# Kernel tuning notes

Measured on AMD Instinct MI355X. Metric: run time of the kernel, lower is better.

## Reference

```python
import jax, jax.numpy as jnp
import numpy as np

B, C, H, W = 8, 256, 64, 64
CI = 128  # inter_channels
EPS = 1e-5

def conv1x1(x, w, b):
    # x:[B,C,H,W], w:[O,C], b:[O] -> [B,O,H,W]
    return jnp.einsum('bchw,oc->bohw', x, w) + b[None, :, None, None]

def maxpool2(t):
    b, c, h, w = t.shape
    return t.reshape(b, c, h // 2, 2, w // 2, 2).max(axis=(3, 5))

def setup_inputs() -> dict:
    key = jax.random.key(0)
    ks = jax.random.split(key, 11)
    s_in = 1.0 / np.sqrt(C)
    s_ci = 1.0 / np.sqrt(CI)
    return {
        'x':        jax.random.normal(ks[0], (B, C, H, W), jnp.float32),
        'g_w':      jax.random.normal(ks[1], (CI, C), jnp.float32) * s_in,
        'g_b':      jax.random.normal(ks[2], (CI,), jnp.float32) * s_in,
        'theta_w':  jax.random.normal(ks[3], (CI, C), jnp.float32) * s_in,
        'theta_b':  jax.random.normal(ks[4], (CI,), jnp.float32) * s_in,
        'phi_w':    jax.random.normal(ks[5], (CI, C), jnp.float32) * s_in,
        'phi_b':    jax.random.normal(ks[6], (CI,), jnp.float32) * s_in,
        'w_w':      jax.random.normal(ks[7], (C, CI), jnp.float32) * s_ci,
        'w_b':      jax.random.normal(ks[8], (C,), jnp.float32) * s_ci,
        'bn_gamma': jax.random.normal(ks[9], (C,), jnp.float32) * 0.1 + 1.0,
        'bn_beta':  jax.random.normal(ks[10], (C,), jnp.float32) * 0.1,
    }

def reference(x, g_w, g_b, theta_w, theta_b, phi_w, phi_b, w_w, w_b, bn_gamma, bn_beta):
    b, c, h, w = x.shape
    n = h * w
    # g and phi are sub-sampled with 2x2 max pool -> Ns = n // 4
    g_x = maxpool2(conv1x1(x, g_w, g_b)).reshape(b, CI, -1)      # [B,CI,Ns]
    g_x = g_x.transpose(0, 2, 1)                                  # [B,Ns,CI]
    theta_x = conv1x1(x, theta_w, theta_b).reshape(b, CI, n)
    theta_x = theta_x.transpose(0, 2, 1)                          # [B,N,CI]
    phi_x = maxpool2(conv1x1(x, phi_w, phi_b)).reshape(b, CI, -1)  # [B,CI,Ns]
    f = jnp.einsum('bnc,bcm->bnm', theta_x, phi_x)                # [B,N,Ns] (no 1/sqrt(d) scale, faithful)
    f_div_c = jax.nn.softmax(f, axis=-1)
    y = jnp.einsum('bnm,bmc->bnc', f_div_c, g_x)                  # [B,N,CI]
    y = y.transpose(0, 2, 1).reshape(b, CI, h, w)
    wy = conv1x1(y, w_w, w_b)                                     # [B,C,H,W]
    # BatchNorm2d in training mode: batch stats over (B,H,W)
    mean = wy.mean(axis=(0, 2, 3), keepdims=True)
    var = wy.var(axis=(0, 2, 3), keepdims=True)
    wy_bn = (wy - mean) * jax.lax.rsqrt(var + EPS)
    wy_bn = wy_bn * bn_gamma[None, :, None, None] + bn_beta[None, :, None, None]
    return wy_bn + x
```

## Files before the change

### kernel.cpp

```cpp
#include <hip/hip_runtime.h>
#include <hip/hip_bf16.h>
#include <hip/hip_fp16.h>
#include <math.h>

#define B 8
#define C 256
#define HH 64
#define WW 64
#define NN 4096
#define CI 128
#define NS 1024
#define EPS 1e-5f

typedef __attribute__((ext_vector_type(8))) _Float16 f16x8;
typedef __attribute__((ext_vector_type(4))) float f32x4;

static __device__ __forceinline__ unsigned short f2h_bits(float f) {
    return __half_as_ushort(__float2half(f));
}
static __device__ __forceinline__ float h2f(unsigned short u) {
    return __half2float(__ushort_as_half(u));
}

__global__ __launch_bounds__(256) void k_xt(const float* __restrict__ x,
        unsigned short* __restrict__ xh,
        const float* __restrict__ tw, const float* __restrict__ pw,
        const float* __restrict__ gw, const float* __restrict__ ww,
        unsigned short* __restrict__ wh) {
    int tid = threadIdx.x;
    if (blockIdx.x == 64) {
        int inst = blockIdx.y * B + blockIdx.z;
        int base = inst * 4096;
        #pragma unroll
        for (int k = 0; k < 16; ++k) {
            int idx = base + tid + k * 256;
            int sel = idx >> 15, off = idx & 32767;
            const float* src = (sel == 0) ? tw : (sel == 1) ? pw : (sel == 2) ? gw : ww;
            wh[idx] = f2h_bits(src[off]);
        }
        return;
    }
    __shared__ float s_t[64 * 65];
    int n0 = blockIdx.x * 64;
    int c0 = blockIdx.y * 64;
    int b  = blockIdx.z;
    #pragma unroll
    for (int k = 0; k < 16; ++k) {
        int idx = tid + k * 256;
        int cl = idx >> 6, nl = idx & 63;
        s_t[cl * 65 + nl] = x[((size_t)b * C + c0 + cl) * NN + n0 + nl];
    }
    __syncthreads();
    #pragma unroll
    for (int k = 0; k < 8; ++k) {
        int idx = tid + k * 256;
        int nl = idx >> 5, cp = (idx & 31) * 2;
        ushort2 o;
        o.x = f2h_bits(s_t[cp * 65 + nl]);
        o.y = f2h_bits(s_t[(cp + 1) * 65 + nl]);
        *(ushort2*)&xh[((size_t)b * NN + n0 + nl) * C + c0 + cp] = o;
    }
}

__global__ __launch_bounds__(512) void k_convs(const unsigned short* __restrict__ xh,
        const unsigned short* __restrict__ twh, const unsigned short* __restrict__ pwh,
        const unsigned short* __restrict__ gwh,
        const float* __restrict__ tb, const float* __restrict__ pb, const float* __restrict__ gb_,
        unsigned short* __restrict__ theta, unsigned short* __restrict__ phi,
        unsigned short* __restrict__ gout) {
    int blk = blockIdx.x;
    int b   = blk >> 5;
    int mh  = blk & 31;
    int tid = threadIdx.x;
    int lane = tid & 63, wv = tid >> 6;
    int lr = lane & 15, lh = lane >> 4;
    int wn = wv & 3, wc = wv >> 2;
    size_t row0 = (size_t)blk * 128;

    f32x4 accT[8];
    f32x4 aP0[4], aP1[4], aG0[4], aG1[4];
    #pragma unroll
    for (int i = 0; i < 8; ++i) accT[i] = (f32x4){0,0,0,0};
    #pragma unroll
    for (int i = 0; i < 4; ++i) {
        aP0[i] = (f32x4){0,0,0,0}; aP1[i] = (f32x4){0,0,0,0};
        aG0[i] = (f32x4){0,0,0,0}; aG1[i] = (f32x4){0,0,0,0};
    }

    const unsigned short* ap0 = xh + (row0 + wn * 16 + lr) * C + lh * 8;
    const unsigned short* ap1 = ap0 + (size_t)64 * C;
    #pragma unroll
    for (int kc = 0; kc < 8; ++kc) {
        f16x8 a0 = *(const f16x8*)(ap0 + kc * 32);
        f16x8 a1 = *(const f16x8*)(ap1 + kc * 32);
        f16x8 aT = (wv < 4) ? a0 : a1;
        #pragma unroll
        for (int ct = 0; ct < 8; ++ct) {
            f16x8 bt_ = *(const f16x8*)&twh[(ct * 16 + lr) * C + kc * 32 + lh * 8];
            accT[ct] = __builtin_amdgcn_mfma_f32_16x16x32_f16(aT, bt_, accT[ct], 0, 0, 0);
        }
        #pragma unroll
        for (int ct = 0; ct < 4; ++ct) {
            int wrow = (wc * 64 + ct * 16 + lr) * C + kc * 32 + lh * 8;
            f16x8 bp = *(const f16x8*)&pwh[wrow];
            f16x8 bg = *(const f16x8*)&gwh[wrow];
            aP0[ct] = __builtin_amdgcn_mfma_f32_16x16x32_f16(a0, bp, aP0[ct], 0, 0, 0);
            aP1[ct] = __builtin_amdgcn_mfma_f32_16x16x32_f16(a1, bp, aP1[ct], 0, 0, 0);
            aG0[ct] = __builtin_amdgcn_mfma_f32_16x16x32_f16(a0, bg, aG0[ct], 0, 0, 0);
            aG1[ct] = __builtin_amdgcn_mfma_f32_16x16x32_f16(a1, bg, aG1[ct], 0, 0, 0);
        }
    }
    #pragma unroll
    for (int ct = 0; ct < 8; ++ct) {
        int ci = ct * 16 + lr;
        float bias = tb[ci];
        #pragma unroll
        for (int r = 0; r < 4; ++r)
            theta[(row0 + wv * 16 + lh * 4 + r) * CI + ci] = f2h_bits(accT[ct][r] + bias);
    }
    #pragma unroll
    for (int ct = 0; ct < 4; ++ct) {
        int ci = wc * 64 + ct * 16 + lr;
        float biasP = pb[ci], biasG = gb_[ci];
        #pragma unroll
        for (int j = 0; j < 2; ++j) {
            int m = mh * 32 + wn * 8 + lh * 2 + j;
            float vP = fmaxf(fmaxf(aP0[ct][2*j], aP0[ct][2*j+1]),
                             fmaxf(aP1[ct][2*j], aP1[ct][2*j+1])) + biasP;
            float vG = fmaxf(fmaxf(aG0[ct][2*j], aG0[ct][2*j+1]),
                             fmaxf(aG1[ct][2*j], aG1[ct][2*j+1])) + biasG;
            phi[((size_t)b * NS + m) * CI + ci]  = f2h_bits(vP);
            gout[((size_t)b * CI + ci) * NS + m] = f2h_bits(vG);
        }
    }
}

#define SPH 136
#define SG  72
#define SP  68
__global__ __launch_bounds__(256) void k_attn_mfma(const unsigned short* __restrict__ theta,
        const unsigned short* __restrict__ phi, const unsigned short* __restrict__ g,
        unsigned short* __restrict__ y) {
    __shared__ unsigned short s_ph[2][64 * SPH];
    __shared__ unsigned short s_g[2][128 * SG];
    __shared__ unsigned short s_p[64 * SP];
    int rb = blockIdx.x;
    int b  = blockIdx.y;
    int tid = threadIdx.x;
    int lane = tid & 63, wv = tid >> 6;
    int lr = lane & 15, lh = lane >> 4;
    int row0 = rb * 64;
    int wrow = wv * 16;

    f16x8 a_th[4];
    {
        const unsigned short* tp = theta + ((size_t)b * NN + row0 + wrow + lr) * CI + lh * 8;
        #pragma unroll
        for (int kc = 0; kc < 4; ++kc) a_th[kc] = *(const f16x8*)(tp + kc * 32);
    }

    const ushort4* phsrc = (const ushort4*)(phi + (size_t)b * NS * CI);
    const ushort4* gsrc  = (const ushort4*)(g + (size_t)b * CI * NS);

    f32x4 yacc[8];
    #pragma unroll
    for (int i = 0; i < 8; ++i) yacc[i] = (f32x4){0.f, 0.f, 0.f, 0.f};
    float mrun[4] = {-1e30f, -1e30f, -1e30f, -1e30f};
    float lrun[4] = {0.f, 0.f, 0.f, 0.f};

    ushort4 rph[8], rg[8];
    #pragma unroll
    for (int k = 0; k < 8; ++k) {
        int t = tid + k * 256;
        rph[k] = phsrc[(t >> 5) * 32 + (t & 31)];
        rg[k]  = gsrc[(t >> 4) * 256 + (t & 15)];
    }
    #pragma unroll
    for (int k = 0; k < 8; ++k) {
        int t = tid + k * 256;
        *(ushort4*)&s_ph[0][(t >> 5) * SPH + (t & 31) * 4] = rph[k];
        *(ushort4*)&s_g[0][(t >> 4) * SG + (t & 15) * 4]   = rg[k];
    }
    __syncthreads();
    int cur = 0;

    for (int mt = 0; mt < 16; ++mt) {
        if (mt < 15) {
            #pragma unroll
            for (int k = 0; k < 8; ++k) {
                int t = tid + k * 256;
                rph[k] = phsrc[((mt + 1) * 64 + (t >> 5)) * 32 + (t & 31)];
                rg[k]  = gsrc[(t >> 4) * 256 + (mt + 1) * 16 + (t & 15)];
            }
        }
        const unsigned short* ph = s_ph[cur];
        const unsigned short* sg_ = s_g[cur];

        f32x4 S[4];
        #pragma unroll
        for (int nt = 0; nt < 4; ++nt) S[nt] = (f32x4){0.f, 0.f, 0.f, 0.f};
        __builtin_amdgcn_s_setprio(1);
        #pragma unroll
        for (int nt = 0; nt < 4; ++nt) {
            #pragma unroll
            for (int kc = 0; kc < 4; ++kc) {
                f16x8 bf = *(const f16x8*)&ph[(nt * 16 + lr) * SPH + kc * 32 + lh * 8];
                S[nt] = __builtin_amdgcn_mfma_f32_16x16x32_f16(a_th[kc], bf, S[nt], 0, 0, 0);
            }
        }
        __builtin_amdgcn_s_setprio(0);

        float rmax[4], rs[4], scale[4];
        #pragma unroll
        for (int r = 0; r < 4; ++r)
            rmax[r] = fmaxf(fmaxf(S[0][r], S[1][r]), fmaxf(S[2][r], S[3][r]));
        #pragma unroll
        for (int s = 1; s < 16; s <<= 1) {
            #pragma unroll
            for (int r = 0; r < 4; ++r) rmax[r] = fmaxf(rmax[r], __shfl_xor(rmax[r], s));
        }
        #pragma unroll
        for (int r = 0; r < 4; ++r) {
            float mnew = fmaxf(mrun[r], rmax[r]);
            scale[r] = __expf(mrun[r] - mnew);
            mrun[r] = mnew;
            rs[r] = 0.f;
        }
        #pragma unroll
        for (int nt = 0; nt < 4; ++nt) {
            #pragma unroll
            for (int r = 0; r < 4; ++r) {
                float e = __expf(S[nt][r] - mrun[r]);
                S[nt][r] = e;
                rs[r] += e;
            }
        }
        #pragma unroll
        for (int s = 1; s < 16; s <<= 1) {
            #pragma unroll
            for (int r = 0; r < 4; ++r) rs[r] += __shfl_xor(rs[r], s);
        }
        #pragma unroll
        for (int r = 0; r < 4; ++r) lrun[r] = lrun[r] * scale[r] + rs[r];
        #pragma unroll
        for (int i = 0; i < 8; ++i) {
            #pragma unroll
            for (int r = 0; r < 4; ++r) yacc[i][r] *= scale[r];
        }
        #pragma unroll
        for (int nt = 0; nt < 4; ++nt) {
            #pragma unroll
            for (int r = 0; r < 4; ++r)
                s_p[(wrow + lh * 4 + r) * SP + nt * 16 + lr] = f2h_bits(S[nt][r]);
        }

        f16x8 a_p[2];
        #pragma unroll
        for (int kc = 0; kc < 2; ++kc)
            a_p[kc] = *(const f16x8*)&s_p[(wrow + lr) * SP + kc * 32 + lh * 8];
        __builtin_amdgcn_s_setprio(1);
        #pragma unroll
        for (int ct = 0; ct < 8; ++ct) {
            #pragma unroll
            for (int kc = 0; kc < 2; ++kc) {
                f16x8 bg = *(const f16x8*)&sg_[(ct * 16 + lr) * SG + kc * 32 + lh * 8];
                yacc[ct] = __builtin_amdgcn_mfma_f32_16x16x32_f16(a_p[kc], bg, yacc[ct], 0, 0, 0);
            }
        }
        __builtin_amdgcn_s_setprio(0);

        if (mt < 15) {
            int nxt = cur ^ 1;
            #pragma unroll
            for (int k = 0; k < 8; ++k) {
                int t = tid + k * 256;
                *(ushort4*)&s_ph[nxt][(t >> 5) * SPH + (t & 31) * 4] = rph[k];
                *(ushort4*)&s_g[nxt][(t >> 4) * SG + (t & 15) * 4]   = rg[k];
            }
            __syncthreads();
            cur = nxt;
        }
    }

    float inv[4];
    #pragma unroll
    for (int r = 0; r < 4; ++r) inv[r] = 1.f / lrun[r];
    #pragma unroll
    for (int ct = 0; ct < 8; ++ct) {
        #pragma unroll
        for (int r = 0; r < 4; ++r)
            y[((size_t)b * NN + row0 + wrow + lh * 4 + r) * CI + ct * 16 + lr] =
                f2h_bits(yacc[ct][r] * inv[r]);
    }
}

__global__ __launch_bounds__(256) void k_wconv(const unsigned short* __restrict__ y,
        const unsigned short* __restrict__ wwh, const float* __restrict__ wb,
        unsigned short* __restrict__ wyh, float* __restrict__ psum, float* __restrict__ psq) {
    int blk = blockIdx.x;
    int b   = blk >> 6;
    int nloc = (blk & 63) * 64;
    int tid = threadIdx.x;
    int lane = tid & 63, wv = tid >> 6;
    int lr = lane & 15, lh = lane >> 4;

    f32x4 acc[4][4];
    #pragma unroll
    for (int i = 0; i < 4; ++i)
        #pragma unroll
        for (int j = 0; j < 4; ++j) acc[i][j] = (f32x4){0.f, 0.f, 0.f, 0.f};

    const unsigned short* yb = y + ((size_t)b * NN + nloc) * CI;
    #pragma unroll
    for (int kc = 0; kc < 4; ++kc) {
        f16x8 a[4], bf[4];
        #pragma unroll
        for (int at = 0; at < 4; ++at)
            a[at] = *(const f16x8*)&wwh[(wv * 64 + at * 16 + lr) * CI + kc * 32 + lh * 8];
        #pragma unroll
        for (int bt = 0; bt < 4; ++bt)
            bf[bt] = *(const f16x8*)&yb[(size_t)(bt * 16 + lr) * CI + kc * 32 + lh * 8];
        #pragma unroll
        for (int at = 0; at < 4; ++at)
            #pragma unroll
            for (int bt = 0; bt < 4; ++bt)
                acc[at][bt] = __builtin_amdgcn_mfma_f32_16x16x32_f16(a[at], bf[bt], acc[at][bt], 0, 0, 0);
    }
    #pragma unroll
    for (int at = 0; at < 4; ++at) {
        #pragma unroll
        for (int r = 0; r < 4; ++r) {
            int co = wv * 64 + at * 16 + lh * 4 + r;
            float bias = wb[co];
            unsigned short* wp = wyh + ((size_t)b * C + co) * NN + nloc;
            float s = 0.f, q = 0.f;
            #pragma unroll
            for (int bt = 0; bt < 4; ++bt) {
                float v = acc[at][bt][r] + bias;
                wp[bt * 16 + lr] = f2h_bits(v);
                s += v;
                q = fmaf(v, v, q);
            }
            #pragma unroll
            for (int o = 1; o < 16; o <<= 1) {
                s += __shfl_xor(s, o);
                q += __shfl_xor(q, o);
            }
            if (lr == 0) {
                psum[co * 512 + blk] = s;
                psq[co * 512 + blk]  = q;
            }
        }
    }
}

__global__ __launch_bounds__(64) void k_stats_r(const float* __restrict__ psum,
        const float* __restrict__ psq, float* __restrict__ stats) {
    int c = blockIdx.x;
    int lane = threadIdx.x;
    float s = 0.f, q = 0.f;
    #pragma unroll
    for (int k = 0; k < 8; ++k) {
        s += psum[c * 512 + lane + k * 64];
        q += psq[c * 512 + lane + k * 64];
    }
    #pragma unroll
    for (int o = 32; o >= 1; o >>= 1) {
        s += __shfl_down(s, o);
        q += __shfl_down(q, o);
    }
    if (lane == 0) { stats[c] = s; stats[256 + c] = q; }
}

__global__ __launch_bounds__(256) void k_bn_out(const unsigned short* __restrict__ wyh,
        const float* __restrict__ x, const float* __restrict__ stats,
        const float* __restrict__ gamma, const float* __restrict__ beta,
        float* __restrict__ out) {
    size_t t = (size_t)blockIdx.x * 256 + threadIdx.x;
    size_t base = t * 8;
    int c = (int)((base >> 12) & 255);
    float mean = stats[c] * (1.f / 32768.f);
    float var  = stats[256 + c] * (1.f / 32768.f) - mean * mean;
    float sc = gamma[c] * rsqrtf(var + EPS);
    float sh = beta[c] - mean * sc;
    ushort4 w0 = *(const ushort4*)&wyh[base];
    ushort4 w1 = *(const ushort4*)&wyh[base + 4];
    float4 x0 = *(const float4*)&x[base];
    float4 x1 = *(const float4*)&x[base + 4];
    float4 o0, o1;
    o0.x = fmaf(h2f(w0.x), sc, sh) + x0.x;
    o0.y = fmaf(h2f(w0.y), sc, sh) + x0.y;
    o0.z = fmaf(h2f(w0.z), sc, sh) + x0.z;
    o0.w = fmaf(h2f(w0.w), sc, sh) + x0.w;
    o1.x = fmaf(h2f(w1.x), sc, sh) + x1.x;
    o1.y = fmaf(h2f(w1.y), sc, sh) + x1.y;
    o1.z = fmaf(h2f(w1.z), sc, sh) + x1.z;
    o1.w = fmaf(h2f(w1.w), sc, sh) + x1.w;
    *(float4*)&out[base]     = o0;
    *(float4*)&out[base + 4] = o1;
}

extern "C" void kernel_launch(void* const* d_in, const int* in_sizes, int n_in,
                              void* d_out, int out_size, void* d_ws, size_t ws_size,
                              hipStream_t stream) {
    const float* x    = (const float*)d_in[0];
    const float* g_w  = (const float*)d_in[1];
    const float* g_b  = (const float*)d_in[2];
    const float* th_w = (const float*)d_in[3];
    const float* th_b = (const float*)d_in[4];
    const float* ph_w = (const float*)d_in[5];
    const float* ph_b = (const float*)d_in[6];
    const float* w_w  = (const float*)d_in[7];
    const float* w_b  = (const float*)d_in[8];
    const float* bn_g = (const float*)d_in[9];
    const float* bn_b = (const float*)d_in[10];
    float* out = (float*)d_out;

    char* w0 = (char*)d_ws;
    unsigned short* xh    = (unsigned short*)w0;
    unsigned short* theta = (unsigned short*)(w0 + 16777216);
    unsigned short* wh    = (unsigned short*)(w0 + 25165824);
    unsigned short* twh   = wh;
    unsigned short* pwh   = wh + 32768;
    unsigned short* gwh   = wh + 65536;
    unsigned short* wwh   = wh + 98304;
    unsigned short* phi   = (unsigned short*)(w0 + 25427968);
    unsigned short* gx    = (unsigned short*)(w0 + 27525120);
    unsigned short* yh    = (unsigned short*)(w0 + 29622272);
    unsigned short* wyh   = (unsigned short*)(w0 + 38010880);
    float*          psum  = (float*)(w0 + 54788096);
    float*          psq   = (float*)(w0 + 55312384);
    float*          stats = (float*)(w0 + 55836672);

    k_xt<<<dim3(65, 4, B), 256, 0, stream>>>(x, xh, th_w, ph_w, g_w, w_w, wh);
    k_convs<<<256, 512, 0, stream>>>(xh, twh, pwh, gwh, th_b, ph_b, g_b, theta, phi, gx);
    k_attn_mfma<<<dim3(64, B), 256, 0, stream>>>(theta, phi, gx, yh);
    k_wconv<<<512, 256, 0, stream>>>(yh, wwh, w_b, wyh, psum, psq);
    k_stats_r<<<256, 64, 0, stream>>>(psum, psq, stats);
    k_bn_out<<<4096, 256, 0, stream>>>(wyh, x, stats, bn_g, bn_b, out);
}
```

Measured before the change: 131.8 us.

## Rewrite attention kernel with 32x32 MFMA, split-KV waves and lazy rescaling

The attention kernel now uses 32x32x16 MFMA tiles with the score matrix computed transposed (phi as A, theta as B). The KV sequence is split between two wave pairs whose partial softmax states are merged through LDS at the end. LDS tiles use XOR swizzling instead of padding. Online-softmax rescaling is skipped unless the running max grows by more than a threshold, which reduces per-step VALU and shuffle work. The new scheme adds a final merge pass, and the deferred rescale can lose fp16 headroom if scores move a lot.

```diff
diff --git a/kernel.cpp b/kernel.cpp
--- a/kernel.cpp
+++ b/kernel.cpp
@@ -11,15 +11,23 @@
 #define CI 128
 #define NS 1024
 #define EPS 1e-5f
+#define THR 8.0f
 
 typedef __attribute__((ext_vector_type(8))) _Float16 f16x8;
 typedef __attribute__((ext_vector_type(4))) float f32x4;
+typedef __attribute__((ext_vector_type(16))) float f32x16;
 
 static __device__ __forceinline__ unsigned short f2h_bits(float f) {
     return __half_as_ushort(__float2half(f));
 }
 static __device__ __forceinline__ float h2f(unsigned short u) {
     return __half2float(__ushort_as_half(u));
+}
+static __device__ __forceinline__ unsigned pk2(float a, float b) {
+    typedef __fp16 fp16x2_t __attribute__((ext_vector_type(2)));
+    union { fp16x2_t h; unsigned u; } cv;
+    cv.h = __builtin_amdgcn_cvt_pkrtz(a, b);
+    return cv.u;
 }
 
 __global__ __launch_bounds__(256) void k_xt(const float* __restrict__ x,
@@ -135,162 +143,185 @@
     }
 }
 
-#define SPH 136
-#define SG  72
-#define SP  68
 __global__ __launch_bounds__(256) void k_attn_mfma(const unsigned short* __restrict__ theta,
         const unsigned short* __restrict__ phi, const unsigned short* __restrict__ g,
         unsigned short* __restrict__ y) {
-    __shared__ unsigned short s_ph[2][64 * SPH];
-    __shared__ unsigned short s_g[2][128 * SG];
-    __shared__ unsigned short s_p[64 * SP];
-    int rb = blockIdx.x;
-    int b  = blockIdx.y;
+    __shared__ unsigned lds_u32[20480];
+    int bid = blockIdx.x;
+    int b   = bid & 7;
+    int rb  = bid >> 3;
     int tid = threadIdx.x;
-    int lane = tid & 63, wv = tid >> 6;
-    int lr = lane & 15, lh = lane >> 4;
+    int lane = tid & 63;
+    int wv  = tid >> 6;
+    int h   = wv & 1;
+    int s   = wv >> 1;
+    int l31 = lane & 31;
+    int lh2 = lane >> 5;
+    int xr  = (lane & 7) << 2;
     int row0 = rb * 64;
-    int wrow = wv * 16;
-
-    f16x8 a_th[4];
+
+    const unsigned phb = s * 4096;
+    const unsigned gbb = 8192 + s * 4096;
+    const unsigned pbb = 16384 + wv * 1024;
+
+    f16x8 b_th[8];
     {
-        const unsigned short* tp = theta + ((size_t)b * NN + row0 + wrow + lr) * CI + lh * 8;
-        #pragma unroll
-        for (int kc = 0; kc < 4; ++kc) a_th[kc] = *(const f16x8*)(tp + kc * 32);
-    }
-
-    const ushort4* phsrc = (const ushort4*)(phi + (size_t)b * NS * CI);
-    const ushort4* gsrc  = (const ushort4*)(g + (size_t)b * CI * NS);
-
-    f32x4 yacc[8];
-    #pragma unroll
-    for (int i = 0; i < 8; ++i) yacc[i] = (f32x4){0.f, 0.f, 0.f, 0.f};
-    float mrun[4] = {-1e30f, -1e30f, -1e30f, -1e30f};
-    float lrun[4] = {0.f, 0.f, 0.f, 0.f};
-
-    ushort4 rph[8], rg[8];
-    #pragma unroll
-    for (int k = 0; k < 8; ++k) {
-        int t = tid + k * 256;
-        rph[k] = phsrc[(t >> 5) * 32 + (t & 31)];
-        rg[k]  = gsrc[(t >> 4) * 256 + (t & 15)];
-    }
-    #pragma unroll
-    for (int k = 0; k < 8; ++k) {
-        int t = tid + k * 256;
-        *(ushort4*)&s_ph[0][(t >> 5) * SPH + (t & 31) * 4] = rph[k];
-        *(ushort4*)&s_g[0][(t >> 4) * SG + (t & 15) * 4]   = rg[k];
-    }
+        const unsigned short* tp = theta + ((size_t)b * NN + row0 + h * 32 + l31) * CI + lh2 * 8;
+        #pragma unroll
+        for (int kc = 0; kc < 8; ++kc)
+            b_th[kc] = *(const f16x8*)(tp + kc * 16);
+    }
+
+    const unsigned short* phsrc = phi + (size_t)b * NS * CI;
+    const unsigned short* gsrc  = g + (size_t)b * CI * NS;
+    int tl = tid & 127;
+
+    uint4 rph[8], rg[8];
+    auto issue = [&](int mt) {
+        #pragma unroll
+        for (int k = 0; k < 8; ++k) {
+            int rowm = k * 8 + (tl >> 4);
+            rph[k] = *(const uint4*)(phsrc + (size_t)(mt * 64 + rowm) * CI + (tl & 15) * 8);
+            int ci = k * 16 + (tl >> 3);
+            rg[k]  = *(const uint4*)(gsrc + (size_t)ci * NS + mt * 64 + (tl & 7) * 8);
+        }
+    };
+    auto commit = [&]() {
+        #pragma unroll
+        for (int k = 0; k < 8; ++k) {
+            int rowm = k * 8 + (tl >> 4);
+            *(uint4*)&lds_u32[phb + rowm * 64 + (((tl & 15) * 4) ^ ((rowm & 7) << 2))] = rph[k];
+            int ci = k * 16 + (tl >> 3);
+            *(uint4*)&lds_u32[gbb + ci * 32 + (((tl & 7) * 4) ^ ((ci & 7) << 2))] = rg[k];
+        }
+    };
+
+    f32x16 yacc[4];
+    #pragma unroll
+    for (int cc = 0; cc < 4; ++cc)
+        #pragma unroll
+        for (int i = 0; i < 16; ++i) yacc[cc][i] = 0.f;
+    float mrun = -1e30f, lrun = 0.f;
+
+    issue(s * 8);
+    commit();
     __syncthreads();
-    int cur = 0;
-
-    for (int mt = 0; mt < 16; ++mt) {
-        if (mt < 15) {
-            #pragma unroll
-            for (int k = 0; k < 8; ++k) {
-                int t = tid + k * 256;
-                rph[k] = phsrc[((mt + 1) * 64 + (t >> 5)) * 32 + (t & 31)];
-                rg[k]  = gsrc[(t >> 4) * 256 + (mt + 1) * 16 + (t & 15)];
-            }
-        }
-        const unsigned short* ph = s_ph[cur];
-        const unsigned short* sg_ = s_g[cur];
-
-        f32x4 S[4];
-        #pragma unroll
-        for (int nt = 0; nt < 4; ++nt) S[nt] = (f32x4){0.f, 0.f, 0.f, 0.f};
+
+    for (int step = 0; step < 8; ++step) {
+        if (step < 7) issue(s * 8 + step + 1);
+
+        f32x16 S0, S1;
+        #pragma unroll
+        for (int i = 0; i < 16; ++i) { S0[i] = 0.f; S1[i] = 0.f; }
         __builtin_amdgcn_s_setprio(1);
         #pragma unroll
-        for (int nt = 0; nt < 4; ++nt) {
+        for (int kc = 0; kc < 8; ++kc) {
+            unsigned dc = (unsigned)((kc * 8 + lh2 * 4) ^ xr);
+            f16x8 a0 = *(const f16x8*)&lds_u32[phb + l31 * 64 + dc];
+            f16x8 a1 = *(const f16x8*)&lds_u32[phb + (32 + l31) * 64 + dc];
+            S0 = __builtin_amdgcn_mfma_f32_32x32x16_f16(a0, b_th[kc], S0, 0, 0, 0);
+            S1 = __builtin_amdgcn_mfma_f32_32x32x16_f16(a1, b_th[kc], S1, 0, 0, 0);
+        }
+        __builtin_amdgcn_s_setprio(0);
+
+        float tmax = S0[0];
+        #pragma unroll
+        for (int i = 1; i < 16; ++i) tmax = fmaxf(tmax, S0[i]);
+        #pragma unroll
+        for (int i = 0; i < 16; ++i) tmax = fmaxf(tmax, S1[i]);
+        tmax = fmaxf(tmax, __shfl_xor(tmax, 32));
+        if (__ballot(tmax > mrun + THR)) {
+            float mnew = fmaxf(mrun, tmax);
+            float scl = __expf(mrun - mnew);
+            mrun = mnew;
+            lrun *= scl;
+            #pragma unroll
+            for (int r = 0; r < 16; ++r) {
+                float sr = __shfl(scl, (lane & 32) + ((r & 3) + 8 * (r >> 2) + 4 * lh2));
+                #pragma unroll
+                for (int cc = 0; cc < 4; ++cc) yacc[cc][r] *= sr;
+            }
+        }
+        float rsum = 0.f;
+        #pragma unroll
+        for (int i = 0; i < 16; ++i) { S0[i] = __expf(S0[i] - mrun); rsum += S0[i]; }
+        #pragma unroll
+        for (int i = 0; i < 16; ++i) { S1[i] = __expf(S1[i] - mrun); rsum += S1[i]; }
+        rsum += __shfl_xor(rsum, 32);
+        lrun += rsum;
+
+        unsigned prow = pbb + (unsigned)l31 * 32;
+        #pragma unroll
+        for (int q = 0; q < 4; ++q) {
+            uint2 w0; w0.x = pk2(S0[4*q], S0[4*q+1]); w0.y = pk2(S0[4*q+2], S0[4*q+3]);
+            *(uint2*)&lds_u32[prow + (unsigned)((q * 4 + 2 * lh2) ^ xr)] = w0;
+            uint2 w1; w1.x = pk2(S1[4*q], S1[4*q+1]); w1.y = pk2(S1[4*q+2], S1[4*q+3]);
+            *(uint2*)&lds_u32[prow + (unsigned)((16 + q * 4 + 2 * lh2) ^ xr)] = w1;
+        }
+
+        f16x8 a_p[4];
+        #pragma unroll
+        for (int kc = 0; kc < 4; ++kc)
+            a_p[kc] = *(const f16x8*)&lds_u32[prow + (unsigned)((kc * 8 + lh2 * 4) ^ xr)];
+        __builtin_amdgcn_s_setprio(1);
+        #pragma unroll
+        for (int cc = 0; cc < 4; ++cc) {
             #pragma unroll
             for (int kc = 0; kc < 4; ++kc) {
-                f16x8 bf = *(const f16x8*)&ph[(nt * 16 + lr) * SPH + kc * 32 + lh * 8];
-                S[nt] = __builtin_amdgcn_mfma_f32_16x16x32_f16(a_th[kc], bf, S[nt], 0, 0, 0);
+                f16x8 bg = *(const f16x8*)&lds_u32[gbb + (unsigned)(cc * 32 + l31) * 32
+                                                  + (unsigned)((kc * 8 + lh2 * 4) ^ xr)];
+                yacc[cc] = __builtin_amdgcn_mfma_f32_32x32x16_f16(a_p[kc], bg, yacc[cc], 0, 0, 0);
             }
         }
         __builtin_amdgcn_s_setprio(0);
 
-        float rmax[4], rs[4], scale[4];
-        #pragma unroll
-        for (int r = 0; r < 4; ++r)
-            rmax[r] = fmaxf(fmaxf(S[0][r], S[1][r]), fmaxf(S[2][r], S[3][r]));
-        #pragma unroll
-        for (int s = 1; s < 16; s <<= 1) {
-            #pragma unroll
-            for (int r = 0; r < 4; ++r) rmax[r] = fmaxf(rmax[r], __shfl_xor(rmax[r], s));
-        }
-        #pragma unroll
-        for (int r = 0; r < 4; ++r) {
-            float mnew = fmaxf(mrun[r], rmax[r]);
-            scale[r] = __expf(mrun[r] - mnew);
-            mrun[r] = mnew;
-            rs[r] = 0.f;
-        }
-        #pragma unroll
-        for (int nt = 0; nt < 4; ++nt) {
-            #pragma unroll
-            for (int r = 0; r < 4; ++r) {
-                float e = __expf(S[nt][r] - mrun[r]);
-                S[nt][r] = e;
-                rs[r] += e;
-            }
-        }
-        #pragma unroll
-        for (int s = 1; s < 16; s <<= 1) {
-            #pragma unroll
-            for (int r = 0; r < 4; ++r) rs[r] += __shfl_xor(rs[r], s);
-        }
-        #pragma unroll
-        for (int r = 0; r < 4; ++r) lrun[r] = lrun[r] * scale[r] + rs[r];
-        #pragma unroll
-        for (int i = 0; i < 8; ++i) {
-            #pragma unroll
-            for (int r = 0; r < 4; ++r) yacc[i][r] *= scale[r];
-        }
-        #pragma unroll
-        for (int nt = 0; nt < 4; ++nt) {
-            #pragma unroll
-            for (int r = 0; r < 4; ++r)
-                s_p[(wrow + lh * 4 + r) * SP + nt * 16 + lr] = f2h_bits(S[nt][r]);
-        }
-
-        f16x8 a_p[2];
-        #pragma unroll
-        for (int kc = 0; kc < 2; ++kc)
-            a_p[kc] = *(const f16x8*)&s_p[(wrow + lr) * SP + kc * 32 + lh * 8];
-        __builtin_amdgcn_s_setprio(1);
-        #pragma unroll
-        for (int ct = 0; ct < 8; ++ct) {
-            #pragma unroll
-            for (int kc = 0; kc < 2; ++kc) {
-                f16x8 bg = *(const f16x8*)&sg_[(ct * 16 + lr) * SG + kc * 32 + lh * 8];
-                yacc[ct] = __builtin_amdgcn_mfma_f32_16x16x32_f16(a_p[kc], bg, yacc[ct], 0, 0, 0);
-            }
-        }
-        __builtin_amdgcn_s_setprio(0);
-
-        if (mt < 15) {
-            int nxt = cur ^ 1;
-            #pragma unroll
-            for (int k = 0; k < 8; ++k) {
-                int t = tid + k * 256;
-                *(ushort4*)&s_ph[nxt][(t >> 5) * SPH + (t & 31) * 4] = rph[k];
-                *(ushort4*)&s_g[nxt][(t >> 4) * SG + (t & 15) * 4]   = rg[k];
-            }
+        __syncthreads();
+        if (step < 7) {
+            commit();
             __syncthreads();
-            cur = nxt;
-        }
-    }
-
-    float inv[4];
-    #pragma unroll
-    for (int r = 0; r < 4; ++r) inv[r] = 1.f / lrun[r];
-    #pragma unroll
-    for (int ct = 0; ct < 8; ++ct) {
-        #pragma unroll
-        for (int r = 0; r < 4; ++r)
-            y[((size_t)b * NN + row0 + wrow + lh * 4 + r) * CI + ct * 16 + lr] =
-                f2h_bits(yacc[ct][r] * inv[r]);
+        }
+    }
+
+    float* cf = (float*)lds_u32;
+    if (s == 1) {
+        if (lh2 == 0) {
+            cf[8192 + h * 32 + l31] = mrun;
+            cf[8256 + h * 32 + l31] = lrun;
+        }
+        #pragma unroll
+        for (int r = 0; r < 16; ++r) {
+            int ny = (r & 3) + 8 * (r >> 2) + 4 * lh2;
+            #pragma unroll
+            for (int cc = 0; cc < 4; ++cc)
+                cf[h * 4096 + ny * 128 + cc * 32 + l31] = yacc[cc][r];
+        }
+    }
+    __syncthreads();
+    if (s == 0) {
+        float m1 = cf[8192 + h * 32 + l31];
+        float l1 = cf[8256 + h * 32 + l31];
+        float M  = fmaxf(mrun, m1);
+        float a  = __expf(mrun - M), bt = __expf(m1 - M);
+        float L  = a * lrun + bt * l1;
+        if (lh2 == 0) {
+            cf[8320 + h * 32 + l31] = a / L;
+            cf[8384 + h * 32 + l31] = bt / L;
+        }
+    }
+    __syncthreads();
+    if (s == 0) {
+        #pragma unroll
+        for (int r = 0; r < 16; ++r) {
+            int ny = (r & 3) + 8 * (r >> 2) + 4 * lh2;
+            float far = cf[8320 + h * 32 + ny];
+            float fbr = cf[8384 + h * 32 + ny];
+            unsigned short* yp = y + ((size_t)b * NN + row0 + h * 32 + ny) * CI + l31;
+            #pragma unroll
+            for (int cc = 0; cc < 4; ++cc) {
+                float y1 = cf[h * 4096 + ny * 128 + cc * 32 + l31];
+                yp[cc * 32] = f2h_bits(far * yacc[cc][r] + fbr * y1);
+            }
+        }
     }
 }
 
@@ -333,21 +364,21 @@
             int co = wv * 64 + at * 16 + lh * 4 + r;
             float bias = wb[co];
             unsigned short* wp = wyh + ((size_t)b * C + co) * NN + nloc;
-            float s = 0.f, q = 0.f;
+            float sv = 0.f, q = 0.f;
             #pragma unroll
             for (int bt = 0; bt < 4; ++bt) {
                 float v = acc[at][bt][r] + bias;
                 wp[bt * 16 + lr] = f2h_bits(v);
-                s += v;
+                sv += v;
                 q = fmaf(v, v, q);
             }
             #pragma unroll
             for (int o = 1; o < 16; o <<= 1) {
-                s += __shfl_xor(s, o);
-                q += __shfl_xor(q, o);
+                sv += __shfl_xor(sv, o);
+                q  += __shfl_xor(q, o);
             }
             if (lr == 0) {
-                psum[co * 512 + blk] = s;
+                psum[co * 512 + blk] = sv;
                 psq[co * 512 + blk]  = q;
             }
         }
@@ -434,7 +465,7 @@
 
     k_xt<<<dim3(65, 4, B), 256, 0, stream>>>(x, xh, th_w, ph_w, g_w, w_w, wh);
     k_convs<<<256, 512, 0, stream>>>(xh, twh, pwh, gwh, th_b, ph_b, g_b, theta, phi, gx);
-    k_attn_mfma<<<dim3(64, B), 256, 0, stream>>>(theta, phi, gx, yh);
+    k_attn_mfma<<<512, 256, 0, stream>>>(theta, phi, gx, yh);
     k_wconv<<<512, 256, 0, stream>>>(yh, wwh, w_b, wyh, psum, psq);
     k_stats_r<<<256, 64, 0, stream>>>(psum, psq, stats);
     k_bn_out<<<4096, 256, 0, stream>>>(wyh, x, stats, bn_g, bn_b, out);
```

New measurement: 207.1 us. 57.2% more time.

## Split attention over key dimension into two halves, merge partials in wconv

Applied to the files above, without the earlier changes.

The attention kernel now splits the 1024 key positions across two grid slices (split-K, flash-decoding style). Each slice writes unnormalized partial outputs plus running max and sum, and the W-conv kernel merges the two halves while loading its B operand. The goal is to double the block count from 512 to 1024 so the 256 CUs are better filled. In exchange it drops the register-prefetch double buffering and setprio, adds partial-output traffic and merge arithmetic, and reuses the xh workspace region for the partials.

```diff
diff --git a/kernel.cpp b/kernel.cpp
--- a/kernel.cpp
+++ b/kernel.cpp
@@ -137,15 +137,16 @@
 
 #define SPH 136
 #define SG  72
-#define SP  68
+#define SP  72
 __global__ __launch_bounds__(256) void k_attn_mfma(const unsigned short* __restrict__ theta,
         const unsigned short* __restrict__ phi, const unsigned short* __restrict__ g,
-        unsigned short* __restrict__ y) {
-    __shared__ unsigned short s_ph[2][64 * SPH];
-    __shared__ unsigned short s_g[2][128 * SG];
+        unsigned short* __restrict__ yp, float2* __restrict__ ml) {
+    __shared__ unsigned short s_ph[64 * SPH];
+    __shared__ unsigned short s_g[128 * SG];
     __shared__ unsigned short s_p[64 * SP];
     int rb = blockIdx.x;
     int b  = blockIdx.y;
+    int sx = blockIdx.z;
     int tid = threadIdx.x;
     int lane = tid & 63, wv = tid >> 6;
     int lr = lane & 15, lh = lane >> 4;
@@ -159,56 +160,46 @@
         for (int kc = 0; kc < 4; ++kc) a_th[kc] = *(const f16x8*)(tp + kc * 32);
     }
 
-    const ushort4* phsrc = (const ushort4*)(phi + (size_t)b * NS * CI);
-    const ushort4* gsrc  = (const ushort4*)(g + (size_t)b * CI * NS);
-
     f32x4 yacc[8];
     #pragma unroll
     for (int i = 0; i < 8; ++i) yacc[i] = (f32x4){0.f, 0.f, 0.f, 0.f};
     float mrun[4] = {-1e30f, -1e30f, -1e30f, -1e30f};
     float lrun[4] = {0.f, 0.f, 0.f, 0.f};
 
-    ushort4 rph[8], rg[8];
-    #pragma unroll
-    for (int k = 0; k < 8; ++k) {
-        int t = tid + k * 256;
-        rph[k] = phsrc[(t >> 5) * 32 + (t & 31)];
-        rg[k]  = gsrc[(t >> 4) * 256 + (t & 15)];
-    }
-    #pragma unroll
-    for (int k = 0; k < 8; ++k) {
-        int t = tid + k * 256;
-        *(ushort4*)&s_ph[0][(t >> 5) * SPH + (t & 31) * 4] = rph[k];
-        *(ushort4*)&s_g[0][(t >> 4) * SG + (t & 15) * 4]   = rg[k];
-    }
-    __syncthreads();
-    int cur = 0;
-
-    for (int mt = 0; mt < 16; ++mt) {
-        if (mt < 15) {
+    for (int t = 0; t < 8; ++t) {
+        int mt = sx * 8 + t;
+        __syncthreads();
+        {
+            const ushort4* src = (const ushort4*)(phi + ((size_t)b * NS + mt * 64) * CI);
             #pragma unroll
             for (int k = 0; k < 8; ++k) {
-                int t = tid + k * 256;
-                rph[k] = phsrc[((mt + 1) * 64 + (t >> 5)) * 32 + (t & 31)];
-                rg[k]  = gsrc[(t >> 4) * 256 + (mt + 1) * 16 + (t & 15)];
-            }
-        }
-        const unsigned short* ph = s_ph[cur];
-        const unsigned short* sg_ = s_g[cur];
+                int tt = tid + k * 256;
+                int r = tt >> 5, cq = tt & 31;
+                ushort4 vv = src[r * 32 + cq];
+                *(ushort4*)&s_ph[r * SPH + cq * 4] = vv;
+            }
+            const ushort4* sg = (const ushort4*)(g + (size_t)b * CI * NS);
+            #pragma unroll
+            for (int k = 0; k < 8; ++k) {
+                int tt = tid + k * 256;
+                int ci = tt >> 4, cq = tt & 15;
+                ushort4 vv = sg[ci * 256 + mt * 16 + cq];
+                *(ushort4*)&s_g[ci * SG + cq * 4] = vv;
+            }
+        }
+        __syncthreads();
 
         f32x4 S[4];
         #pragma unroll
         for (int nt = 0; nt < 4; ++nt) S[nt] = (f32x4){0.f, 0.f, 0.f, 0.f};
-        __builtin_amdgcn_s_setprio(1);
         #pragma unroll
         for (int nt = 0; nt < 4; ++nt) {
             #pragma unroll
             for (int kc = 0; kc < 4; ++kc) {
-                f16x8 bf = *(const f16x8*)&ph[(nt * 16 + lr) * SPH + kc * 32 + lh * 8];
+                f16x8 bf = *(const f16x8*)&s_ph[(nt * 16 + lr) * SPH + kc * 32 + lh * 8];
                 S[nt] = __builtin_amdgcn_mfma_f32_16x16x32_f16(a_th[kc], bf, S[nt], 0, 0, 0);
             }
         }
-        __builtin_amdgcn_s_setprio(0);
 
         float rmax[4], rs[4], scale[4];
         #pragma unroll
@@ -258,45 +249,36 @@
         #pragma unroll
         for (int kc = 0; kc < 2; ++kc)
             a_p[kc] = *(const f16x8*)&s_p[(wrow + lr) * SP + kc * 32 + lh * 8];
-        __builtin_amdgcn_s_setprio(1);
         #pragma unroll
         for (int ct = 0; ct < 8; ++ct) {
             #pragma unroll
             for (int kc = 0; kc < 2; ++kc) {
-                f16x8 bg = *(const f16x8*)&sg_[(ct * 16 + lr) * SG + kc * 32 + lh * 8];
+                f16x8 bg = *(const f16x8*)&s_g[(ct * 16 + lr) * SG + kc * 32 + lh * 8];
                 yacc[ct] = __builtin_amdgcn_mfma_f32_16x16x32_f16(a_p[kc], bg, yacc[ct], 0, 0, 0);
             }
         }
-        __builtin_amdgcn_s_setprio(0);
-
-        if (mt < 15) {
-            int nxt = cur ^ 1;
-            #pragma unroll
-            for (int k = 0; k < 8; ++k) {
-                int t = tid + k * 256;
-                *(ushort4*)&s_ph[nxt][(t >> 5) * SPH + (t & 31) * 4] = rph[k];
-                *(ushort4*)&s_g[nxt][(t >> 4) * SG + (t & 15) * 4]   = rg[k];
-            }
-            __syncthreads();
-            cur = nxt;
-        }
-    }
-
-    float inv[4];
-    #pragma unroll
-    for (int r = 0; r < 4; ++r) inv[r] = 1.f / lrun[r];
+    }
+
+    size_t pbase = ((size_t)(sx * B + b) * NN + row0 + wrow);
     #pragma unroll
     for (int ct = 0; ct < 8; ++ct) {
         #pragma unroll
         for (int r = 0; r < 4; ++r)
-            y[((size_t)b * NN + row0 + wrow + lh * 4 + r) * CI + ct * 16 + lr] =
-                f2h_bits(yacc[ct][r] * inv[r]);
-    }
-}
-
-__global__ __launch_bounds__(256) void k_wconv(const unsigned short* __restrict__ y,
-        const unsigned short* __restrict__ wwh, const float* __restrict__ wb,
-        unsigned short* __restrict__ wyh, float* __restrict__ psum, float* __restrict__ psq) {
+            yp[(pbase + lh * 4 + r) * CI + ct * 16 + lr] = f2h_bits(yacc[ct][r]);
+    }
+    if (lr == 0) {
+        #pragma unroll
+        for (int r = 0; r < 4; ++r) {
+            float2 v; v.x = mrun[r]; v.y = lrun[r];
+            ml[pbase + lh * 4 + r] = v;
+        }
+    }
+}
+
+__global__ __launch_bounds__(256) void k_wconv(const unsigned short* __restrict__ yp,
+        const float2* __restrict__ ml, const unsigned short* __restrict__ wwh,
+        const float* __restrict__ wb, unsigned short* __restrict__ wyh,
+        float* __restrict__ psum, float* __restrict__ psq) {
     int blk = blockIdx.x;
     int b   = blk >> 6;
     int nloc = (blk & 63) * 64;
@@ -310,7 +292,23 @@
         #pragma unroll
         for (int j = 0; j < 4; ++j) acc[i][j] = (f32x4){0.f, 0.f, 0.f, 0.f};
 
-    const unsigned short* yb = y + ((size_t)b * NN + nloc) * CI;
+    const unsigned short* y0b = yp + ((size_t)b * NN + nloc) * CI;
+    const unsigned short* y1b = yp + ((size_t)(B + b) * NN + nloc) * CI;
+    const float2* ml0 = ml + ((size_t)b * NN + nloc);
+    const float2* ml1 = ml + ((size_t)(B + b) * NN + nloc);
+
+    float a0v[4], a1v[4];
+    #pragma unroll
+    for (int bt = 0; bt < 4; ++bt) {
+        int n = bt * 16 + lr;
+        float2 p0 = ml0[n], p1 = ml1[n];
+        float M = fmaxf(p0.x, p1.x);
+        float e0 = __expf(p0.x - M), e1 = __expf(p1.x - M);
+        float L = e0 * p0.y + e1 * p1.y;
+        a0v[bt] = e0 / L;
+        a1v[bt] = e1 / L;
+    }
+
     #pragma unroll
     for (int kc = 0; kc < 4; ++kc) {
         f16x8 a[4], bf[4];
@@ -318,8 +316,16 @@
         for (int at = 0; at < 4; ++at)
             a[at] = *(const f16x8*)&wwh[(wv * 64 + at * 16 + lr) * CI + kc * 32 + lh * 8];
         #pragma unroll
-        for (int bt = 0; bt < 4; ++bt)
-            bf[bt] = *(const f16x8*)&yb[(size_t)(bt * 16 + lr) * CI + kc * 32 + lh * 8];
+        for (int bt = 0; bt < 4; ++bt) {
+            size_t off = (size_t)(bt * 16 + lr) * CI + kc * 32 + lh * 8;
+            f16x8 u0 = *(const f16x8*)&y0b[off];
+            f16x8 u1 = *(const f16x8*)&y1b[off];
+            f16x8 v;
+            #pragma unroll
+            for (int i = 0; i < 8; ++i)
+                v[i] = (_Float16)(a0v[bt] * (float)u0[i] + a1v[bt] * (float)u1[i]);
+            bf[bt] = v;
+        }
         #pragma unroll
         for (int at = 0; at < 4; ++at)
             #pragma unroll
@@ -333,21 +339,21 @@
             int co = wv * 64 + at * 16 + lh * 4 + r;
             float bias = wb[co];
             unsigned short* wp = wyh + ((size_t)b * C + co) * NN + nloc;
-            float s = 0.f, q = 0.f;
+            float sv = 0.f, q = 0.f;
             #pragma unroll
             for (int bt = 0; bt < 4; ++bt) {
                 float v = acc[at][bt][r] + bias;
                 wp[bt * 16 + lr] = f2h_bits(v);
-                s += v;
+                sv += v;
                 q = fmaf(v, v, q);
             }
             #pragma unroll
             for (int o = 1; o < 16; o <<= 1) {
-                s += __shfl_xor(s, o);
-                q += __shfl_xor(q, o);
+                sv += __shfl_xor(sv, o);
+                q  += __shfl_xor(q, o);
             }
             if (lr == 0) {
-                psum[co * 512 + blk] = s;
+                psum[co * 512 + blk] = sv;
                 psq[co * 512 + blk]  = q;
             }
         }
@@ -418,6 +424,7 @@
 
     char* w0 = (char*)d_ws;
     unsigned short* xh    = (unsigned short*)w0;
+    unsigned short* yp    = (unsigned short*)w0;
     unsigned short* theta = (unsigned short*)(w0 + 16777216);
     unsigned short* wh    = (unsigned short*)(w0 + 25165824);
     unsigned short* twh   = wh;
@@ -426,16 +433,16 @@
     unsigned short* wwh   = wh + 98304;
     unsigned short* phi   = (unsigned short*)(w0 + 25427968);
     unsigned short* gx    = (unsigned short*)(w0 + 27525120);
-    unsigned short* yh    = (unsigned short*)(w0 + 29622272);
     unsigned short* wyh   = (unsigned short*)(w0 + 38010880);
     float*          psum  = (float*)(w0 + 54788096);
     float*          psq   = (float*)(w0 + 55312384);
     float*          stats = (float*)(w0 + 55836672);
+    float2*         ml    = (float2*)(w0 + 55840768);
 
     k_xt<<<dim3(65, 4, B), 256, 0, stream>>>(x, xh, th_w, ph_w, g_w, w_w, wh);
     k_convs<<<256, 512, 0, stream>>>(xh, twh, pwh, gwh, th_b, ph_b, g_b, theta, phi, gx);
-    k_attn_mfma<<<dim3(64, B), 256, 0, stream>>>(theta, phi, gx, yh);
-    k_wconv<<<512, 256, 0, stream>>>(yh, wwh, w_b, wyh, psum, psq);
+    k_attn_mfma<<<dim3(64, B, 2), 256, 0, stream>>>(theta, phi, gx, yp, ml);
+    k_wconv<<<512, 256, 0, stream>>>(yp, ml, wwh, w_b, wyh, psum, psq);
     k_stats_r<<<256, 64, 0, stream>>>(psum, psq, stats);
     k_bn_out<<<4096, 256, 0, stream>>>(wyh, x, stats, bn_g, bn_b, out);
 }
```

Result: slower. 192.6 us (+46.1%).
